# Kernel tuning notes

Measured on AMD Instinct MI355X. Metric: run time of the kernel, lower is better.

The kernel has to match this reference:

```python
import jax, jax.numpy as jnp
import numpy as np

B, N, C = 16384, 4, 512
H = 8
HD = C // H
WIN = 2
SCALE = HD ** -0.5
HID = 2048


def _rel_pos_index(w):
    # same construction as the torch buffer, done in numpy (constant)
    coords = np.stack(np.meshgrid(np.arange(w), np.arange(w), indexing='ij'))  # [2,w,w]
    flat = coords.reshape(2, -1)                      # [2, w*w]
    rel = flat[:, :, None] - flat[:, None, :]         # [2, N, N]
    rel = rel.transpose(1, 2, 0).astype(np.int64)     # [N, N, 2]
    rel[:, :, 0] += w - 1
    rel[:, :, 1] += w - 1
    rel[:, :, 0] *= 2 * w - 1
    return rel.sum(-1)                                # [N, N]

REL_IDX = _rel_pos_index(WIN)


def setup_inputs() -> dict:
    key = jax.random.key(0)
    ks = jax.random.split(key, 8)
    s = lambda fan: 1.0 / np.sqrt(fan)
    return {
        'x': jax.random.normal(ks[0], (B, N, C), jnp.float32),
        'ln_g': jnp.ones((C,), jnp.float32),
        'ln_b': jnp.zeros((C,), jnp.float32),
        'qkv_w': jax.random.normal(ks[1], (3 * C, C), jnp.float32) * s(C),
        'proj_w': jax.random.normal(ks[2], (C, C), jnp.float32) * s(C),
        'proj_b': jnp.zeros((C,), jnp.float32),
        'rpb_table': jax.random.normal(ks[3], ((2 * WIN - 1) ** 2, H), jnp.float32) * 0.02,
        'fc1_w': jax.random.normal(ks[4], (HID, C), jnp.float32) * s(C),
        'fc1_b': jnp.zeros((HID,), jnp.float32),
        'fc2_w': jax.random.normal(ks[5], (C, HID), jnp.float32) * s(HID),
        'fc2_b': jnp.zeros((C,), jnp.float32),
    }


def _layernorm(x, g, b, eps=1e-5):
    mu = jnp.mean(x, axis=-1, keepdims=True)
    var = jnp.mean(jnp.square(x - mu), axis=-1, keepdims=True)
    return (x - mu) * jax.lax.rsqrt(var + eps) * g + b


def reference(x, ln_g, ln_b, qkv_w, proj_w, proj_b, rpb_table, fc1_w, fc1_b, fc2_w, fc2_b):
    # --- attention branch (pre-norm, shared LayerNorm params) ---
    h = _layernorm(x, ln_g, ln_b)
    qkv = h @ qkv_w.T                                  # [B,N,3C]
    qkv = qkv.reshape(B, N, 3, H, HD).transpose(2, 0, 3, 1, 4)  # [3,B,H,N,HD]
    q, k, v = qkv[0], qkv[1], qkv[2]
    attn = jnp.einsum('bhnd,bhmd->bhnm', q, k) * SCALE  # [B,H,N,N]
    bias = rpb_table[REL_IDX.reshape(-1)].reshape(N, N, H).transpose(2, 0, 1)  # [H,N,N]
    attn = jax.nn.softmax(attn + bias[None], axis=-1)
    o = jnp.einsum('bhnm,bhmd->bhnd', attn, v)          # [B,H,N,HD]
    o = o.transpose(0, 2, 1, 3).reshape(B, N, C)
    o = o @ proj_w.T + proj_b
    x = x + o
    # --- MLP branch (same LayerNorm params reused, as in the torch code) ---
    h = _layernorm(x, ln_g, ln_b)
    h = jax.nn.gelu(h @ fc1_w.T + fc1_b, approximate=False)
    h = h @ fc2_w.T + fc2_b
    return x + h
```

## Files before the change

### kernel.cpp

```cpp
#include <hip/hip_runtime.h>
#include <hip/hip_bf16.h>
#include <math.h>

#define BQ   16384
#define CH   512
#define NH   8
#define HID  2048
#define NTOK (BQ*4)

using bf16 = __hip_bfloat16;
typedef __bf16 bf16x8 __attribute__((ext_vector_type(8)));
typedef float  f32x4  __attribute__((ext_vector_type(4)));

__device__ __forceinline__ void gload16(const void* g, void* l) {
    __builtin_amdgcn_global_load_lds(
        (const __attribute__((address_space(1))) void*)g,
        (__attribute__((address_space(3))) void*)l, 16, 0, 0);
}

__global__ __launch_bounds__(256) void packw(const float* __restrict__ Wsrc,
                                             bf16* __restrict__ out, int N, int K) {
    int q = blockIdx.x * 256 + threadIdx.x;
    int NSk = K >> 5;
    int total = (N >> 8) * NSk * 1024;
    if (q >= total) return;
    int l  = q & 63;
    int jj = (q >> 6) & 1;
    int w  = (q >> 7) & 7;
    int s  = (q >> 10) % NSk;
    int cb = q / (NSk * 1024);
    int row = cb * 256 + w * 32 + jj * 16 + (l >> 2);
    int k   = s * 32 + ((l & 3) ^ ((l >> 3) & 3)) * 8;
    const float* src = Wsrc + (size_t)row * K + k;
    float4 v0 = *(const float4*)src;
    float4 v1 = *(const float4*)(src + 4);
    __align__(16) bf16 t[8];
    t[0] = __float2bfloat16(v0.x); t[1] = __float2bfloat16(v0.y);
    t[2] = __float2bfloat16(v0.z); t[3] = __float2bfloat16(v0.w);
    t[4] = __float2bfloat16(v1.x); t[5] = __float2bfloat16(v1.y);
    t[6] = __float2bfloat16(v1.z); t[7] = __float2bfloat16(v1.w);
    *(uint4*)&out[(size_t)q * 8] = *(const uint4*)t;
}

__global__ __launch_bounds__(256) void ln_kernel(const float* __restrict__ x,
                                                 const float* __restrict__ g,
                                                 const float* __restrict__ b,
                                                 bf16* __restrict__ out) {
    int row  = blockIdx.x * 4 + (threadIdx.x >> 6);
    int lane = threadIdx.x & 63;
    const float* xr = x + (size_t)row * CH;
    int c0 = lane * 8;
    float4 v0 = *(const float4*)&xr[c0];
    float4 v1 = *(const float4*)&xr[c0 + 4];
    float s  = v0.x + v0.y + v0.z + v0.w + v1.x + v1.y + v1.z + v1.w;
    float sq = v0.x*v0.x + v0.y*v0.y + v0.z*v0.z + v0.w*v0.w
             + v1.x*v1.x + v1.y*v1.y + v1.z*v1.z + v1.w*v1.w;
#pragma unroll
    for (int off = 32; off >= 1; off >>= 1) {
        s  += __shfl_xor(s,  off, 64);
        sq += __shfl_xor(sq, off, 64);
    }
    float mu  = s * (1.0f / CH);
    float var = sq * (1.0f / CH) - mu * mu;
    float rs  = rsqrtf(var + 1e-5f);
    float4 g0 = *(const float4*)&g[c0];
    float4 g1 = *(const float4*)&g[c0 + 4];
    float4 b0 = *(const float4*)&b[c0];
    float4 b1 = *(const float4*)&b[c0 + 4];
    __align__(16) bf16 t[8];
    t[0] = __float2bfloat16((v0.x - mu) * rs * g0.x + b0.x);
    t[1] = __float2bfloat16((v0.y - mu) * rs * g0.y + b0.y);
    t[2] = __float2bfloat16((v0.z - mu) * rs * g0.z + b0.z);
    t[3] = __float2bfloat16((v0.w - mu) * rs * g0.w + b0.w);
    t[4] = __float2bfloat16((v1.x - mu) * rs * g1.x + b1.x);
    t[5] = __float2bfloat16((v1.y - mu) * rs * g1.y + b1.y);
    t[6] = __float2bfloat16((v1.z - mu) * rs * g1.z + b1.z);
    t[7] = __float2bfloat16((v1.w - mu) * rs * g1.w + b1.w);
    *(uint4*)&out[(size_t)row * CH + c0] = *(const uint4*)t;
}

template<int EPI>
__global__ __launch_bounds__(512, 2)
void gemm8p(const bf16* __restrict__ A, const bf16* __restrict__ Bp,
            int M, int N, int K, int nbx,
            const float* __restrict__ bias,
            const float* resid, float* outF, bf16* __restrict__ outB) {
    __shared__ __align__(16) char lds[131072];
    const int tid  = threadIdx.x;
    const int w    = tid >> 6;
    const int lane = tid & 63;

    const int nb  = gridDim.x;
    const int id  = blockIdx.x;
    const int swz = (id & 7) * (nb >> 3) + (id >> 3);
    const int bx  = swz % nbx, by = swz / nbx;
    const int bm = by * 256, bn = bx * 256;
    const int wr = w >> 2;
    const int wc = w & 3;
    const int NSk = K >> 5;

    const int rl  = lane >> 2;
    const int kpe = ((lane & 3) ^ ((lane >> 3) & 3)) * 8;
    const bf16* gA0 = A + (size_t)(bm + w * 32 + rl) * K + kpe;
    const bf16* gA1 = gA0 + (size_t)16 * K;
    const bf16* gB = Bp + (size_t)(bn >> 8) * NSk * 8192 + w * 1024 + lane * 8;

    const int kslot = ((lane >> 4) ^ ((lane >> 1) & 3));
    const int aoff = (wr * 128 + (lane & 15)) * 64 + kslot * 16;
    const int boff = 16384 + (wc * 64 + (lane & 15)) * 64 + kslot * 16;

    f32x4 acc[8][4] = {};
    bf16x8 av0[8], av1[8], b01_0[2], b01_1[2], b23_0[2], b23_1[2];

    auto stageA = [&](int s) {
        char* base = (char*)lds + (s & 3) * 32768;
        gload16(gA0 + (size_t)s * 32, base + w * 2048);
        gload16(gA1 + (size_t)s * 32, base + w * 2048 + 1024);
    };
    auto stageB = [&](int s) {
        char* base = (char*)lds + (s & 3) * 32768;
        gload16(gB + (size_t)s * 8192,       base + 16384 + w * 2048);
        gload16(gB + (size_t)s * 8192 + 512, base + 16384 + w * 2048 + 1024);
    };

#define RD_AV(AV, SLOT) { const char* _b = (const char*)lds + (size_t)((SLOT) & 3) * 32768; \
    _Pragma("unroll") for (int _m = 0; _m < 8; ++_m)                                         \
        AV[_m] = *(const bf16x8*)(_b + aoff + _m * 1024); }
#define RD_B2(BV, SLOT, OFF) { const char* _b = (const char*)lds + (size_t)((SLOT) & 3) * 32768; \
    BV[0] = *(const bf16x8*)(_b + boff + (OFF));                                                 \
    BV[1] = *(const bf16x8*)(_b + boff + (OFF) + 1024); }
#define MF16(AV, BV, N0) { __builtin_amdgcn_s_setprio(1);                                    \
    _Pragma("unroll") for (int _m = 0; _m < 8; ++_m) {                                       \
        acc[_m][N0]     = __builtin_amdgcn_mfma_f32_16x16x32_bf16(AV[_m], BV[0], acc[_m][N0],     0, 0, 0); \
        acc[_m][N0 + 1] = __builtin_amdgcn_mfma_f32_16x16x32_bf16(AV[_m], BV[1], acc[_m][N0 + 1], 0, 0, 0); } \
    __builtin_amdgcn_s_setprio(0); }
#define WAITV(n) asm volatile("s_waitcnt vmcnt(" #n ")" ::: "memory")
#define SBAR()   __builtin_amdgcn_s_barrier()

    stageA(0); stageB(0); stageA(1); stageB(1); stageA(2); stageB(2);
    WAITV(8);
    SBAR();
    RD_AV(av0, 0); RD_B2(b01_0, 0, 0); RD_B2(b23_0, 0, 2048);

    for (int s = 0; s < NSk - 2; s += 2) {
        WAITV(4); SBAR();
        RD_AV(av1, s + 1); RD_B2(b01_1, s + 1, 0);
        if (s + 3 < NSk) stageA(s + 3);
        MF16(av0, b01_0, 0);
        SBAR();
        RD_B2(b23_1, s + 1, 2048);
        if (s + 3 < NSk) stageB(s + 3);
        MF16(av0, b23_0, 2);
        WAITV(4); SBAR();
        RD_AV(av0, s + 2); RD_B2(b01_0, s + 2, 0);
        if (s + 4 < NSk) stageA(s + 4);
        MF16(av1, b01_1, 0);
        SBAR();
        RD_B2(b23_0, s + 2, 2048);
        if (s + 4 < NSk) stageB(s + 4);
        MF16(av1, b23_1, 2);
    }
    WAITV(0); SBAR();
    RD_AV(av1, NSk - 1); RD_B2(b01_1, NSk - 1, 0);
    MF16(av0, b01_0, 0);
    SBAR();
    RD_B2(b23_1, NSk - 1, 2048);
    MF16(av0, b23_0, 2);
    MF16(av1, b01_1, 0);
    MF16(av1, b23_1, 2);
#undef RD_AV
#undef RD_B2
#undef MF16
#undef WAITV
#undef SBAR

    const int erow0 = bm + wr * 128 + (lane >> 4) * 4;
    const int ecol0 = bn + wc * 64 + (lane & 15);
#pragma unroll
    for (int m = 0; m < 8; ++m) {
#pragma unroll
        for (int n = 0; n < 4; ++n) {
            int col = ecol0 + n * 16;
#pragma unroll
            for (int r = 0; r < 4; ++r) {
                int row = erow0 + m * 16 + r;
                size_t idx = (size_t)row * N + col;
                float v = acc[m][n][r];
                if (EPI == 0) {
                    outB[idx] = __float2bfloat16(v);
                } else if (EPI == 1) {
                    outF[idx] = v + bias[col] + resid[idx];
                } else {
                    float t = v + bias[col];
                    float u = 0.7978845608f * t * (1.0f + 0.044715f * t * t);
                    float e = __expf(2.0f * u);
                    float th = 1.0f - 2.0f / (e + 1.0f);
                    outB[idx] = __float2bfloat16(0.5f * t * (1.0f + th));
                }
            }
        }
    }
}

__global__ __launch_bounds__(256)
void attn_kernel(const bf16* __restrict__ qkv, const float* __restrict__ rpb,
                 bf16* __restrict__ o) {
    __shared__ __align__(16) bf16 sT[4 * 1536];
    __shared__ float sS[NH][4][4];
    __shared__ float sP[NH][4][4];
    int b   = blockIdx.x;
    int tid = threadIdx.x;
    const bf16* src = qkv + (size_t)b * (4 * 1536);
#pragma unroll
    for (int it = 0; it < 3; ++it) {
        int e = (it * 256 + tid) * 8;
        *(uint4*)&sT[e] = *(const uint4*)&src[e];
    }
    __syncthreads();
    if (tid < 128) {
        int h = tid >> 4, i = (tid >> 2) & 3, j = tid & 3;
        const bf16* q = &sT[i * 1536 + h * 64];
        const bf16* k = &sT[j * 1536 + 512 + h * 64];
        float acc = 0.f;
#pragma unroll
        for (int d = 0; d < 64; ++d)
            acc += __bfloat162float(q[d]) * __bfloat162float(k[d]);
        int rel = (((i >> 1) - (j >> 1)) + 1) * 3 + (((i & 1) - (j & 1)) + 1);
        sS[h][i][j] = acc * 0.125f + rpb[rel * NH + h];
    }
    __syncthreads();
    if (tid < 32) {
        int h = tid >> 2, i = tid & 3;
        float s0 = sS[h][i][0], s1 = sS[h][i][1], s2 = sS[h][i][2], s3 = sS[h][i][3];
        float mx = fmaxf(fmaxf(s0, s1), fmaxf(s2, s3));
        float e0 = expf(s0 - mx), e1 = expf(s1 - mx), e2 = expf(s2 - mx), e3 = expf(s3 - mx);
        float inv = 1.f / (e0 + e1 + e2 + e3);
        sP[h][i][0] = e0 * inv; sP[h][i][1] = e1 * inv;
        sP[h][i][2] = e2 * inv; sP[h][i][3] = e3 * inv;
    }
    __syncthreads();
    {
        int h = tid >> 5, tl = tid & 31;
        int d = tl * 2;
        const bf16* v = &sT[1024 + h * 64 + d];
#pragma unroll
        for (int i = 0; i < 4; ++i) {
            float p0 = sP[h][i][0], p1 = sP[h][i][1], p2 = sP[h][i][2], p3 = sP[h][i][3];
            float o0 = p0 * __bfloat162float(v[0])        + p1 * __bfloat162float(v[1536])
                     + p2 * __bfloat162float(v[2 * 1536]) + p3 * __bfloat162float(v[3 * 1536]);
            float o1 = p0 * __bfloat162float(v[1])            + p1 * __bfloat162float(v[1536 + 1])
                     + p2 * __bfloat162float(v[2 * 1536 + 1]) + p3 * __bfloat162float(v[3 * 1536 + 1]);
            __hip_bfloat162 pr;
            pr.x = __float2bfloat16(o0);
            pr.y = __float2bfloat16(o1);
            *(__hip_bfloat162*)&o[(size_t)(b * 4 + i) * CH + h * 64 + d] = pr;
        }
    }
}

extern "C" void kernel_launch(void* const* d_in, const int* in_sizes, int n_in,
                              void* d_out, int out_size, void* d_ws, size_t ws_size,
                              hipStream_t stream) {
    const float* x      = (const float*)d_in[0];
    const float* ln_g   = (const float*)d_in[1];
    const float* ln_b   = (const float*)d_in[2];
    const float* qkv_w  = (const float*)d_in[3];
    const float* proj_w = (const float*)d_in[4];
    const float* proj_b = (const float*)d_in[5];
    const float* rpb    = (const float*)d_in[6];
    const float* fc1_w  = (const float*)d_in[7];
    const float* fc1_b  = (const float*)d_in[8];
    const float* fc2_w  = (const float*)d_in[9];
    const float* fc2_b  = (const float*)d_in[10];
    float* out = (float*)d_out;

    char* ws = (char*)d_ws;
    bf16* wQKV  = (bf16*)ws;  ws += (size_t)1536 * 512 * 2;
    bf16* wPROJ = (bf16*)ws;  ws += (size_t)512  * 512 * 2;
    bf16* wFC1  = (bf16*)ws;  ws += (size_t)2048 * 512 * 2;
    bf16* wFC2  = (bf16*)ws;  ws += (size_t)512 * 2048 * 2;
    bf16* hA    = (bf16*)ws;  ws += (size_t)NTOK * 512 * 2;
    bf16* big   = (bf16*)ws;
    const size_t needed = 6291456ull + 67108864ull + 268435456ull;
    if (ws_size < needed) return;

    packw<<<384, 256, 0, stream>>>(qkv_w,  wQKV, 1536, 512);
    packw<<<128, 256, 0, stream>>>(proj_w, wPROJ, 512, 512);
    packw<<<512, 256, 0, stream>>>(fc1_w,  wFC1, 2048, 512);
    packw<<<512, 256, 0, stream>>>(fc2_w,  wFC2, 512, 2048);

    ln_kernel<<<NTOK / 4, 256, 0, stream>>>(x, ln_g, ln_b, hA);
    gemm8p<0><<<dim3(6 * 256), 512, 0, stream>>>(
        hA, wQKV, NTOK, 1536, 512, 6, nullptr, nullptr, nullptr, big);
    attn_kernel<<<BQ, 256, 0, stream>>>(big, rpb, hA);
    gemm8p<1><<<dim3(2 * 256), 512, 0, stream>>>(
        hA, wPROJ, NTOK, 512, 512, 2, proj_b, x, out, nullptr);
    ln_kernel<<<NTOK / 4, 256, 0, stream>>>(out, ln_g, ln_b, hA);
    gemm8p<2><<<dim3(8 * 256), 512, 0, stream>>>(
        hA, wFC1, NTOK, 2048, 512, 8, fc1_b, nullptr, nullptr, big);
    gemm8p<1><<<dim3(2 * 256), 512, 0, stream>>>(
        big, wFC2, NTOK, 512, 2048, 2, fc2_b, out, out, nullptr);
}
```

Before: 846.5 us.

## Restructure GEMM main loop into single-buffered two-phase pipeline with explicit waits

Replaces the double-register-buffered, two-step-unrolled GEMM K loop with a single register set and two phases per K-step (low and high B columns). Each phase issues LDS reads and the next global-to-LDS stage, waits on a barrier plus lgkmcnt(0), then runs its MFMAs. The aim is lower register pressure and tighter control over LDS and vmem wait points. In exchange the LDS-read latency is no longer hidden behind the previous step's MFMAs, and there are more barriers per step.

```diff
diff --git a/kernel.cpp b/kernel.cpp
--- a/kernel.cpp
+++ b/kernel.cpp
@@ -11,6 +11,8 @@
 using bf16 = __hip_bfloat16;
 typedef __bf16 bf16x8 __attribute__((ext_vector_type(8)));
 typedef float  f32x4  __attribute__((ext_vector_type(4)));
+
+#define FENCE() asm volatile("" ::: "memory")
 
 __device__ __forceinline__ void gload16(const void* g, void* l) {
     __builtin_amdgcn_global_load_lds(
@@ -110,69 +112,80 @@
     const int boff = 16384 + (wc * 64 + (lane & 15)) * 64 + kslot * 16;
 
     f32x4 acc[8][4] = {};
-    bf16x8 av0[8], av1[8], b01_0[2], b01_1[2], b23_0[2], b23_1[2];
-
-    auto stageA = [&](int s) {
-        char* base = (char*)lds + (s & 3) * 32768;
-        gload16(gA0 + (size_t)s * 32, base + w * 2048);
-        gload16(gA1 + (size_t)s * 32, base + w * 2048 + 1024);
+    bf16x8 av[8], bl[2], bh[2];
+
+    auto stageA = [&](int t) {
+        char* base = (char*)lds + (t & 3) * 32768;
+        gload16(gA0 + (size_t)t * 32, base + w * 2048);
+        gload16(gA1 + (size_t)t * 32, base + w * 2048 + 1024);
     };
-    auto stageB = [&](int s) {
-        char* base = (char*)lds + (s & 3) * 32768;
-        gload16(gB + (size_t)s * 8192,       base + 16384 + w * 2048);
-        gload16(gB + (size_t)s * 8192 + 512, base + 16384 + w * 2048 + 1024);
+    auto stageB = [&](int t) {
+        char* base = (char*)lds + (t & 3) * 32768 + 16384;
+        gload16(gB + (size_t)t * 8192,       base + w * 2048);
+        gload16(gB + (size_t)t * 8192 + 512, base + w * 2048 + 1024);
     };
 
-#define RD_AV(AV, SLOT) { const char* _b = (const char*)lds + (size_t)((SLOT) & 3) * 32768; \
-    _Pragma("unroll") for (int _m = 0; _m < 8; ++_m)                                         \
-        AV[_m] = *(const bf16x8*)(_b + aoff + _m * 1024); }
-#define RD_B2(BV, SLOT, OFF) { const char* _b = (const char*)lds + (size_t)((SLOT) & 3) * 32768; \
-    BV[0] = *(const bf16x8*)(_b + boff + (OFF));                                                 \
-    BV[1] = *(const bf16x8*)(_b + boff + (OFF) + 1024); }
-#define MF16(AV, BV, N0) { __builtin_amdgcn_s_setprio(1);                                    \
-    _Pragma("unroll") for (int _m = 0; _m < 8; ++_m) {                                       \
-        acc[_m][N0]     = __builtin_amdgcn_mfma_f32_16x16x32_bf16(AV[_m], BV[0], acc[_m][N0],     0, 0, 0); \
-        acc[_m][N0 + 1] = __builtin_amdgcn_mfma_f32_16x16x32_bf16(AV[_m], BV[1], acc[_m][N0 + 1], 0, 0, 0); } \
-    __builtin_amdgcn_s_setprio(0); }
+#define SBAR()  __builtin_amdgcn_s_barrier()
+#define LGKM0() asm volatile("s_waitcnt lgkmcnt(0)" ::: "memory")
 #define WAITV(n) asm volatile("s_waitcnt vmcnt(" #n ")" ::: "memory")
-#define SBAR()   __builtin_amdgcn_s_barrier()
+
+#define PH0(T, DOSTAGE) {                                                    \
+    const char* _b = (const char*)lds + (size_t)((T) & 3) * 32768;           \
+    _Pragma("unroll") for (int _m = 0; _m < 8; ++_m)                         \
+        av[_m] = *(const bf16x8*)(_b + aoff + _m * 1024);                    \
+    bl[0] = *(const bf16x8*)(_b + boff);                                     \
+    bl[1] = *(const bf16x8*)(_b + boff + 1024);                              \
+    if (DOSTAGE) stageA((T) + 3);                                            \
+    SBAR(); LGKM0();                                                         \
+    __builtin_amdgcn_s_setprio(1);                                           \
+    _Pragma("unroll") for (int _m = 0; _m < 8; ++_m) {                       \
+        acc[_m][0] = __builtin_amdgcn_mfma_f32_16x16x32_bf16(av[_m], bl[0], acc[_m][0], 0, 0, 0); \
+        acc[_m][1] = __builtin_amdgcn_mfma_f32_16x16x32_bf16(av[_m], bl[1], acc[_m][1], 0, 0, 0); } \
+    __builtin_amdgcn_s_setprio(0);                                           \
+    SBAR(); }
+
+#define PH1(T, DOSTAGE, VMW) {                                               \
+    const char* _b = (const char*)lds + (size_t)((T) & 3) * 32768;           \
+    bh[0] = *(const bf16x8*)(_b + boff + 2048);                              \
+    bh[1] = *(const bf16x8*)(_b + boff + 3072);                              \
+    if (DOSTAGE) stageB((T) + 3);                                            \
+    SBAR(); LGKM0();                                                         \
+    __builtin_amdgcn_s_setprio(1);                                           \
+    _Pragma("unroll") for (int _m = 0; _m < 8; ++_m) {                       \
+        acc[_m][2] = __builtin_amdgcn_mfma_f32_16x16x32_bf16(av[_m], bh[0], acc[_m][2], 0, 0, 0); \
+        acc[_m][3] = __builtin_amdgcn_mfma_f32_16x16x32_bf16(av[_m], bh[1], acc[_m][3], 0, 0, 0); } \
+    __builtin_amdgcn_s_setprio(0);                                           \
+    VMW;                                                                     \
+    SBAR(); }
 
     stageA(0); stageB(0); stageA(1); stageB(1); stageA(2); stageB(2);
-    WAITV(8);
-    SBAR();
-    RD_AV(av0, 0); RD_B2(b01_0, 0, 0); RD_B2(b23_0, 0, 2048);
-
-    for (int s = 0; s < NSk - 2; s += 2) {
-        WAITV(4); SBAR();
-        RD_AV(av1, s + 1); RD_B2(b01_1, s + 1, 0);
-        if (s + 3 < NSk) stageA(s + 3);
-        MF16(av0, b01_0, 0);
-        SBAR();
-        RD_B2(b23_1, s + 1, 2048);
-        if (s + 3 < NSk) stageB(s + 3);
-        MF16(av0, b23_0, 2);
-        WAITV(4); SBAR();
-        RD_AV(av0, s + 2); RD_B2(b01_0, s + 2, 0);
-        if (s + 4 < NSk) stageA(s + 4);
-        MF16(av1, b01_1, 0);
-        SBAR();
-        RD_B2(b23_0, s + 2, 2048);
-        if (s + 4 < NSk) stageB(s + 4);
-        MF16(av1, b23_1, 2);
-    }
-    WAITV(0); SBAR();
-    RD_AV(av1, NSk - 1); RD_B2(b01_1, NSk - 1, 0);
-    MF16(av0, b01_0, 0);
-    SBAR();
-    RD_B2(b23_1, NSk - 1, 2048);
-    MF16(av0, b23_0, 2);
-    MF16(av1, b01_1, 0);
-    MF16(av1, b23_1, 2);
-#undef RD_AV
-#undef RD_B2
-#undef MF16
+    WAITV(8); SBAR();
+
+    for (int t = 0; t < NSk - 3; ++t) {
+        PH0(t, true);
+        PH1(t, true, WAITV(8));
+    }
+    PH0(NSk - 3, false);
+    PH1(NSk - 3, false, WAITV(4));
+    PH0(NSk - 2, false);
+    PH1(NSk - 2, false, WAITV(0));
+    PH0(NSk - 1, false);
+    {
+        const char* _b = (const char*)lds + (size_t)((NSk - 1) & 3) * 32768;
+        bh[0] = *(const bf16x8*)(_b + boff + 2048);
+        bh[1] = *(const bf16x8*)(_b + boff + 3072);
+        LGKM0();
+#pragma unroll
+        for (int m = 0; m < 8; ++m) {
+            acc[m][2] = __builtin_amdgcn_mfma_f32_16x16x32_bf16(av[m], bh[0], acc[m][2], 0, 0, 0);
+            acc[m][3] = __builtin_amdgcn_mfma_f32_16x16x32_bf16(av[m], bh[1], acc[m][3], 0, 0, 0);
+        }
+    }
+#undef PH0
+#undef PH1
+#undef SBAR
+#undef LGKM0
 #undef WAITV
-#undef SBAR
 
     const int erow0 = bm + wr * 128 + (lane >> 4) * 4;
     const int ecol0 = bn + wc * 64 + (lane & 15);
```

Result: no change. 849.9 us (+0.4%).
